# Optimization experiments

Hardware: AMD Instinct MI355X
Metric: run time of the kernel (lower is better)

## Reference

```python
import jax, jax.numpy as jnp
import numpy as np

B, N, F, H, R = 16, 64, 64, 4, 50
C = F * H  # n_coefficients = n_heads * hidden_features
CUTOFF = 5.0  # ExpNormalSmearing cutoff_upper (cutoff_lower = 0)


def _dense(k, fin, fout):
    s = 1.0 / np.sqrt(fin)
    return jax.random.uniform(k, (fin, fout), jnp.float32, -s, s)


def setup_inputs() -> dict:
    key = jax.random.key(0)
    ks = jax.random.split(key, 20)
    start = float(np.exp(-CUTOFF))
    return {
        "h": jax.random.normal(ks[0], (B, N, F), jnp.float32),
        "x": jax.random.normal(ks[1], (B, N, 3), jnp.float32),
        "v": jax.random.normal(ks[2], (B, N, 3), jnp.float32) * 0.1,
        # edge model (ContinuousFilterConvolutionWithConcatenation)
        "W_in": _dense(ks[3], 2 * F, R), "b_in": jnp.zeros((R,), jnp.float32),
        "rbf_means": jnp.linspace(start, 1.0, R).astype(jnp.float32),
        "rbf_betas": jnp.full((R,), (2.0 / R * (1.0 - start)) ** -2, jnp.float32),
        "W_e1": _dense(ks[4], 2 * F + R + 1, F), "b_e1": jnp.zeros((F,), jnp.float32),
        "W_e2": _dense(ks[5], F, F), "b_e2": jnp.zeros((F,), jnp.float32),
        # semantic attention
        "W_sem": _dense(ks[6], F, H), "b_sem": jnp.zeros((H,), jnp.float32),
        "log_gamma": -jnp.log(jnp.linspace(1.0, 5.0, H)).astype(jnp.float32),
        # spatial attention
        "W_xmix": _dense(ks[7], C, C),
        "W_post1": _dense(ks[8], C, F), "b_post1": jnp.zeros((F,), jnp.float32),
        "W_post2": _dense(ks[9], F, F), "b_post2": jnp.zeros((F,), jnp.float32),
        # node update
        "W_node1": _dense(ks[10], F + C + F, F), "b_node1": jnp.zeros((F,), jnp.float32),
        "W_node2": _dense(ks[11], F, F), "b_node2": jnp.zeros((F,), jnp.float32),
        # velocity update
        "W_vel1": _dense(ks[12], F, F), "b_vel1": jnp.zeros((F,), jnp.float32),
        "W_vel2": _dense(ks[13], F, 1),
        "W_vmix": _dense(ks[14], C, 1),
    }


def reference(h, x, v, W_in, b_in, rbf_means, rbf_betas, W_e1, b_e1, W_e2, b_e2,
              W_sem, b_sem, log_gamma, W_xmix, W_post1, b_post1, W_post2, b_post2,
              W_node1, b_node1, W_node2, b_node2, W_vel1, b_vel1, W_vel2, W_vmix):
    silu = jax.nn.silu
    n = h.shape[-2]
    # pairwise displacement x_j - x_i : (B, N, N, 3)
    x_minus_xt = x[..., None, :, :] - x[..., :, None, :]
    d = jnp.sqrt(jax.nn.relu((x_minus_xt ** 2).sum(-1, keepdims=True)) + 1e-5)  # (B,N,N,1)
    # pairwise node features [h_j, h_i] : (B, N, N, 2F)
    hj = jnp.broadcast_to(h[..., None, :, :], h.shape[:-2] + (n, n, h.shape[-1]))
    hi = jnp.broadcast_to(h[..., :, None, :], hj.shape)
    h_cat = jnp.concatenate([hj, hi], -1)
    # edge model: RBF-smeared continuous-filter conv with concatenation
    h_mid = h_cat @ W_in + b_in  # (B,N,N,R)
    cut = 0.5 * (jnp.cos(d * (jnp.pi / CUTOFF)) + 1.0) * (d < CUTOFF)
    rbf = cut * jnp.exp(-rbf_betas * (jnp.exp(-d) - rbf_means) ** 2)  # (B,N,N,R)
    h_e = jnp.concatenate([h_cat, rbf * h_mid, d], -1)
    h_e = silu(h_e @ W_e1 + b_e1) @ W_e2 + b_e2  # (B,N,N,F)
    # attentions, softmax over neighbor axis (-2), diagonal masked out
    eye = jnp.eye(n, dtype=h.dtype)[:, :, None]
    sem = jax.nn.celu(h_e @ W_sem + b_sem, alpha=2.0) - 1e5 * eye
    sem = jax.nn.softmax(sem, axis=-2)  # (B,N,N,H)
    euc = jax.nn.softmax(-(d + 1e5 * eye) * jnp.exp(log_gamma), axis=-2)  # (B,N,N,H)
    att = euc * sem
    att = att / att.sum(-2, keepdims=True)
    # per-head attention-weighted edge features, flattened (F outer, H inner)
    h_e_att = (h_e[..., :, None] * att[..., None, :]).reshape(att.shape[:-1] + (F * H,))
    # spatial attention on unit displacement vectors
    coeff = jnp.tanh(h_e_att @ W_xmix)  # (B,N,N,C)
    x_hat = x_minus_xt / (d + 1e-5)
    comb = x_hat[..., None, :] * coeff[..., None]  # (B,N,N,C,3)
    comb_sum = comb.mean(axis=-3)  # mean over neighbors -> (B,N,C,3)
    h_comb = (comb_sum ** 2).sum(-1)  # invariant squared norms (B,N,C)
    h_comb = silu(silu(h_comb @ W_post1 + b_post1) @ W_post2 + b_post2)
    # node update (residual)
    h_agg = h_e_att.sum(axis=-2)  # (B,N,C)
    h_out = h + silu(silu(jnp.concatenate([h, h_agg, h_comb], -1) @ W_node1 + b_node1) @ W_node2 + b_node2)
    # equivariant velocity / coordinate update
    delta_v = jnp.einsum('...ijcd,c->...id', comb, W_vmix[:, 0]) / n  # v_mixing + mean over j
    gate = 2.0 * jax.nn.sigmoid(silu(h_out @ W_vel1 + b_vel1) @ W_vel2)  # double_sigmoid, (B,N,1)
    v_out = delta_v + gate * v
    x_out = x + v_out
    return h_out, x_out, v_out
```

## Files before the change

kernel.cpp:

```cpp
#include <hip/hip_runtime.h>
#include <math.h>

#define NB 16
#define NN 64
#define NF 64
#define NH 4
#define NR 50
#define NC 256

typedef __attribute__((ext_vector_type(8))) short short8;
typedef __attribute__((ext_vector_type(4))) float f32x4;

#define WS_WE1R 0
#define WS_WE2  4096
#define WS_WX   9216
#define WS_PO1  74752
#define WS_NO1  91136
#define WS_PO2  115712
#define WS_NO2  119808
#define WS_VE1  123904
#define MID_F   64000
#define E1_F    (MID_F + 131072)
#define HAGG_F  (E1_F + 131072)
#define COMB_F  (HAGG_F + 262144)
#define BS2_F   (COMB_F + 786432)

__device__ __forceinline__ float siluf(float x) { return x / (1.f + __expf(-x)); }
__device__ __forceinline__ float tanhfast(float x) { return 1.f - 2.f / (__expf(2.f * x) + 1.f); }

__device__ __forceinline__ short f2bfs(float f) {
    __bf16 b = (__bf16)f;
    union { __bf16 b; short s; } u; u.b = b; return u.s;
}
__device__ __forceinline__ float bf1(ushort u) {
    union { unsigned u; float f; } c; c.u = ((unsigned)u) << 16; return c.f;
}
__device__ __forceinline__ float bflo(unsigned u) {
    union { unsigned u; float f; } c; c.u = u << 16; return c.f;
}
__device__ __forceinline__ float bfhi(unsigned u) {
    union { unsigned u; float f; } c; c.u = u & 0xFFFF0000u; return c.f;
}

__global__ __launch_bounds__(256)
void prep_kernel(const float* __restrict__ W_e1, const float* __restrict__ b_e1,
                 const float* __restrict__ W_e2, const float* __restrict__ b_e2,
                 const float* __restrict__ W_sem, const float* __restrict__ b_sem,
                 const float* __restrict__ W_xmix,
                 const float* __restrict__ W_post1, const float* __restrict__ W_node1,
                 const float* __restrict__ W_post2, const float* __restrict__ W_node2,
                 const float* __restrict__ W_vel1,
                 const float* __restrict__ h, const float* __restrict__ W_in,
                 const float* __restrict__ b_in,
                 short* __restrict__ wpack, float* __restrict__ mid,
                 float* __restrict__ e1, float* __restrict__ bs2)
{
    int blk = blockIdx.x, t = threadIdx.x;
    if (blk < 63) {
        int s = blk * 256 + t;
        if (s >= 16000) return;
        short8 val;
        if (s < 512) {
            int cl = s & 15, g = (s >> 4) & 3, q = s >> 6;
            int ks = q & 1, nt = q >> 1;
            int c = nt * 16 + cl, k0 = 32 * ks + 8 * g;
#pragma unroll
            for (int i = 0; i < 8; i++) {
                int kr = k0 + i;
                float f = (kr < 50) ? W_e1[(128 + kr) * NF + c] : (kr == 50 ? W_e1[178 * NF + c] : 0.f);
                val[i] = f2bfs(f);
            }
            *(short8*)(&wpack[WS_WE1R + s * 8]) = val;
        } else if (s < 1152) {
            int u = s - 512;
            int cl = u & 15, g = (u >> 4) & 3, q = u >> 6;
            int ks = q & 1, nt = q >> 1;
            int c = nt * 16 + cl, k0 = 32 * ks + 8 * g;
#pragma unroll
            for (int i = 0; i < 8; i++) {
                int k = k0 + i;
                float f;
                if (c < 64) f = W_e2[k * NF + c];
                else {
                    int cc = c - 64;
                    if (cc < 4) {
                        f = 0.f;
                        for (int m = 0; m < 64; m++) f += W_e2[k * NF + m] * W_sem[m * NH + cc];
                    } else f = 0.f;
                }
                val[i] = f2bfs(f);
            }
            *(short8*)(&wpack[WS_WE2 + u * 8]) = val;
        } else if (s < 9344) {
            int u = s - 1152;
            int cl = u & 15, g = (u >> 4) & 3, q = u >> 6;
            int ks = q & 7, wn = q >> 3;
            int c = (wn >> 2) * 64 + (wn & 3) * 16 + cl, k0 = 32 * ks + 8 * g;
#pragma unroll
            for (int i = 0; i < 8; i++) val[i] = f2bfs(W_xmix[(k0 + i) * NC + c]);
            *(short8*)(&wpack[WS_WX + u * 8]) = val;
        } else if (s < 11392) {
            int u = s - 9344;
            int cl = u & 15, g = (u >> 4) & 3, q = u >> 6;
            int ks = q & 7, nt = q >> 3;
            int c = nt * 16 + cl, k0 = 32 * ks + 8 * g;
#pragma unroll
            for (int i = 0; i < 8; i++) val[i] = f2bfs(W_post1[(k0 + i) * NF + c]);
            *(short8*)(&wpack[WS_PO1 + u * 8]) = val;
        } else if (s < 14464) {
            int u = s - 11392;
            int cl = u & 15, g = (u >> 4) & 3, q = u >> 6;
            int ks = q % 12, nt = q / 12;
            int c = nt * 16 + cl, k0 = 32 * ks + 8 * g;
#pragma unroll
            for (int i = 0; i < 8; i++) val[i] = f2bfs(W_node1[(k0 + i) * NF + c]);
            *(short8*)(&wpack[WS_NO1 + u * 8]) = val;
        } else if (s < 14976) {
            int u = s - 14464;
            int cl = u & 15, g = (u >> 4) & 3, q = u >> 6;
            int ks = q & 1, nt = q >> 1;
            int c = nt * 16 + cl, k0 = 32 * ks + 8 * g;
#pragma unroll
            for (int i = 0; i < 8; i++) val[i] = f2bfs(W_post2[(k0 + i) * NF + c]);
            *(short8*)(&wpack[WS_PO2 + u * 8]) = val;
        } else if (s < 15488) {
            int u = s - 14976;
            int cl = u & 15, g = (u >> 4) & 3, q = u >> 6;
            int ks = q & 1, nt = q >> 1;
            int c = nt * 16 + cl, k0 = 32 * ks + 8 * g;
#pragma unroll
            for (int i = 0; i < 8; i++) val[i] = f2bfs(W_node2[(k0 + i) * NF + c]);
            *(short8*)(&wpack[WS_NO2 + u * 8]) = val;
        } else {
            int u = s - 15488;
            int cl = u & 15, g = (u >> 4) & 3, q = u >> 6;
            int ks = q & 1, nt = q >> 1;
            int c = nt * 16 + cl, k0 = 32 * ks + 8 * g;
#pragma unroll
            for (int i = 0; i < 8; i++) val[i] = f2bfs(W_vel1[(k0 + i) * NF + c]);
            *(short8*)(&wpack[WS_VE1 + u * 8]) = val;
        }
    } else if (blk == 63) {
        if (t < 4) {
            float acc = b_sem[t];
            for (int m = 0; m < 64; m++) acc += b_e2[m] * W_sem[m * NH + t];
            bs2[t] = acc;
        }
    } else {
        int node = blk - 64;
        __shared__ float s_hn[64];
        if (t < 64) s_hn[t] = h[node * NF + t];
        __syncthreads();
        if (t < 64) {
            float acc = 0.f;
#pragma unroll 8
            for (int k = 0; k < 64; k++) acc += s_hn[k] * W_e1[k * NF + t];
            e1[node * 128 + t] = acc;
        } else if (t < 128) {
            int f = t - 64;
            float acc = b_e1[f];
#pragma unroll 8
            for (int k = 0; k < 64; k++) acc += s_hn[k] * W_e1[(64 + k) * NF + f];
            e1[node * 128 + 64 + f] = acc;
        } else if (t < 178) {
            int r = t - 128;
            float acc = 0.f;
#pragma unroll 8
            for (int k = 0; k < 64; k++) acc += s_hn[k] * W_in[k * NR + r];
            mid[node * 128 + r] = acc;
        } else if (t >= 192 && t < 242) {
            int r = t - 192;
            float acc = b_in[r];
#pragma unroll 8
            for (int k = 0; k < 64; k++) acc += s_hn[k] * W_in[(64 + k) * NR + r];
            mid[node * 128 + 64 + r] = acc;
        }
    }
}

__global__ __launch_bounds__(64)
void sake_edge_kernel(
    const float* __restrict__ x,
    const float* __restrict__ mid, const float* __restrict__ e1,
    const float* __restrict__ rbf_means, const float* __restrict__ rbf_betas,
    const float* __restrict__ b_e2, const float* __restrict__ bs2,
    const float* __restrict__ log_gamma,
    const short* __restrict__ wpack,
    float* __restrict__ hagg_g, float* __restrict__ comb_g)
{
    const int bi = blockIdx.x;
    const int b  = bi >> 6;
    const int i  = bi & 63;
    const int l  = threadIdx.x;
    const int lr = l & 15, lg = l >> 4;

    __shared__ __align__(16) short s_Ar[8 * 64 * 8];
    __shared__ __align__(16) short s_Au[8 * 64 * 8];
    __shared__ __align__(16) short s_he[64 * 72];
    __shared__ float s_xhat[256];
    __shared__ float s_att[256];

    const short8* A8r  = (const short8*)s_Ar;
    short8*       A8rw = (short8*)s_Ar;
    const short8* A8u  = (const short8*)s_Au;
    const short8* We1p = (const short8*)(wpack + WS_WE1R);
    const short8* We2p = (const short8*)(wpack + WS_WE2);
    const short8* Wxp  = (const short8*)(wpack + WS_WX);

    {
        int j = l;
        float dx = x[(b * NN + j) * 3 + 0] - x[(b * NN + i) * 3 + 0];
        float dy = x[(b * NN + j) * 3 + 1] - x[(b * NN + i) * 3 + 1];
        float dz = x[(b * NN + j) * 3 + 2] - x[(b * NN + i) * 3 + 2];
        float d2 = dx * dx + dy * dy + dz * dz;
        float d  = sqrtf(fmaxf(d2, 0.f) + 1e-5f);
        float inv = 1.f / (d + 1e-5f);
        float4 xh = { dx * inv, dy * inv, dz * inv, d };
        *(float4*)(s_xhat + j * 4) = xh;

        float cut = 0.5f * (__cosf(d * 0.6283185307179586f) + 1.f) * (d < 5.f ? 1.f : 0.f);
        float emd = __expf(-d);
        const float* mj = mid + (size_t)(b * 64 + j) * 128;
        const float* mi = mid + (size_t)(b * 64 + i) * 128 + 64;
#pragma unroll
        for (int g = 0; g < 8; g++) {
            short8 val;
#pragma unroll
            for (int e = 0; e < 8; e++) {
                int r = g * 8 + e;
                float o;
                if (r < 50) {
                    float m = mj[r] + mi[r];
                    float df = emd - rbf_means[r];
                    o = cut * __expf(-rbf_betas[r] * df * df) * m;
                } else if (r == 50) o = d;
                else o = 0.f;
                val[e] = f2bfs(o);
            }
            A8rw[g * 64 + j] = val;
        }
    }

    {
        const float* e1b = e1 + (size_t)b * 64 * 128;
        float e1iv[4];
#pragma unroll
        for (int nt = 0; nt < 4; nt++) e1iv[nt] = e1b[i * 128 + 64 + nt * 16 + lr];
        f32x4 accU[4][4];
#pragma unroll
        for (int jt = 0; jt < 4; jt++)
#pragma unroll
            for (int nt = 0; nt < 4; nt++) {
                int f = nt * 16 + lr;
#pragma unroll
                for (int r = 0; r < 4; r++) {
                    int j = jt * 16 + lg * 4 + r;
                    accU[jt][nt][r] = e1b[j * 128 + f] + e1iv[nt];
                }
            }
#pragma unroll
        for (int ks = 0; ks < 2; ks++) {
            short8 aa[4];
#pragma unroll
            for (int jt = 0; jt < 4; jt++) aa[jt] = A8r[(ks * 4 + lg) * 64 + jt * 16 + lr];
#pragma unroll
            for (int nt = 0; nt < 4; nt++) {
                short8 bb = We1p[(nt * 2 + ks) * 64 + l];
#pragma unroll
                for (int jt = 0; jt < 4; jt++)
                    accU[jt][nt] = __builtin_amdgcn_mfma_f32_16x16x32_bf16(aa[jt], bb, accU[jt][nt], 0, 0, 0);
            }
        }
#pragma unroll
        for (int jt = 0; jt < 4; jt++)
#pragma unroll
            for (int nt = 0; nt < 4; nt++) {
                int f = nt * 16 + lr;
#pragma unroll
                for (int r = 0; r < 4; r++) {
                    int j = jt * 16 + lg * 4 + r;
                    s_Au[((f >> 3) * 64 + j) * 8 + (f & 7)] = f2bfs(siluf(accU[jt][nt][r]));
                }
            }
    }

    f32x4 accS[4];
    {
        f32x4 accE[4][4];
#pragma unroll
        for (int jt = 0; jt < 4; jt++) {
            accS[jt][0] = 0.f; accS[jt][1] = 0.f; accS[jt][2] = 0.f; accS[jt][3] = 0.f;
#pragma unroll
            for (int nt = 0; nt < 4; nt++) {
                accE[jt][nt][0] = 0.f; accE[jt][nt][1] = 0.f; accE[jt][nt][2] = 0.f; accE[jt][nt][3] = 0.f;
            }
        }
#pragma unroll
        for (int ks = 0; ks < 2; ks++) {
            short8 aa[4];
#pragma unroll
            for (int jt = 0; jt < 4; jt++) aa[jt] = A8u[(ks * 4 + lg) * 64 + jt * 16 + lr];
            short8 bb2 = We2p[(8 + ks) * 64 + l];
#pragma unroll
            for (int jt = 0; jt < 4; jt++)
                accS[jt] = __builtin_amdgcn_mfma_f32_16x16x32_bf16(aa[jt], bb2, accS[jt], 0, 0, 0);
#pragma unroll
            for (int nt = 0; nt < 4; nt++) {
                short8 bb = We2p[(nt * 2 + ks) * 64 + l];
#pragma unroll
                for (int jt = 0; jt < 4; jt++)
                    accE[jt][nt] = __builtin_amdgcn_mfma_f32_16x16x32_bf16(aa[jt], bb, accE[jt][nt], 0, 0, 0);
            }
        }
        float be2v[4];
#pragma unroll
        for (int nt = 0; nt < 4; nt++) be2v[nt] = b_e2[nt * 16 + lr];
#pragma unroll
        for (int jt = 0; jt < 4; jt++)
#pragma unroll
            for (int nt = 0; nt < 4; nt++) {
                int f = nt * 16 + lr;
#pragma unroll
                for (int r = 0; r < 4; r++) {
                    int j = jt * 16 + lg * 4 + r;
                    s_he[j * 72 + f] = f2bfs(accE[jt][nt][r] + be2v[nt]);
                }
            }
    }

    {
        float gam = __expf(log_gamma[lr & 3]);
        float bsv = bs2[lr & 3];
        float cel[4][4], dj[4][4];
        float m1 = -1e30f, m2 = -1e30f;
#pragma unroll
        for (int jt = 0; jt < 4; jt++)
#pragma unroll
            for (int r = 0; r < 4; r++) {
                int j = jt * 16 + lg * 4 + r;
                float s = accS[jt][r] + bsv;
                float c = fmaxf(s, 0.f) + fminf(0.f, 2.f * (__expf(0.5f * s) - 1.f));
                float d = s_xhat[j * 4 + 3];
                if (j == i) { c -= 1e5f; d += 1e5f; }
                cel[jt][r] = c; dj[jt][r] = d;
                m1 = fmaxf(m1, c);
                m2 = fmaxf(m2, -d * gam);
            }
        m1 = fmaxf(m1, __shfl_xor(m1, 16)); m1 = fmaxf(m1, __shfl_xor(m1, 32));
        m2 = fmaxf(m2, __shfl_xor(m2, 16)); m2 = fmaxf(m2, __shfl_xor(m2, 32));
        float at[4][4];
        float S1 = 0.f, S2 = 0.f;
#pragma unroll
        for (int jt = 0; jt < 4; jt++)
#pragma unroll
            for (int r = 0; r < 4; r++) {
                float ev1 = __expf(cel[jt][r] - m1);
                float ev2 = __expf(-dj[jt][r] * gam - m2);
                cel[jt][r] = ev1; dj[jt][r] = ev2;
                S1 += ev1; S2 += ev2;
            }
        S1 += __shfl_xor(S1, 16); S1 += __shfl_xor(S1, 32);
        S2 += __shfl_xor(S2, 16); S2 += __shfl_xor(S2, 32);
        float S3 = 0.f;
        float inv12 = 1.f / (S1 * S2);
#pragma unroll
        for (int jt = 0; jt < 4; jt++)
#pragma unroll
            for (int r = 0; r < 4; r++) {
                at[jt][r] = cel[jt][r] * dj[jt][r] * inv12;
                S3 += at[jt][r];
            }
        S3 += __shfl_xor(S3, 16); S3 += __shfl_xor(S3, 32);
        float inv3 = 1.f / S3;
        if (lr < 4) {
#pragma unroll
            for (int jt = 0; jt < 4; jt++)
#pragma unroll
                for (int r = 0; r < 4; r++) {
                    int j = jt * 16 + lg * 4 + r;
                    s_att[j * 4 + lr] = at[jt][r] * inv3;
                }
        }
    }

    {
        float hg0 = 0.f, hg1 = 0.f, hg2 = 0.f, hg3 = 0.f;
#pragma unroll 8
        for (int j = 0; j < 64; j++) {
            float hev = bf1((ushort)s_he[j * 72 + l]);
            float4 at = *(const float4*)(s_att + j * 4);
            hg0 += hev * at.x; hg1 += hev * at.y; hg2 += hev * at.z; hg3 += hev * at.w;
        }
        float4 o = { hg0, hg1, hg2, hg3 };
        *(float4*)(hagg_g + bi * 256 + l * 4) = o;
    }

    {
        short8 fr[4][8];
#pragma unroll
        for (int jt = 0; jt < 4; jt++) {
            int j = jt * 16 + lr;
            float4 a = *(const float4*)(s_att + j * 4);
#pragma unroll
            for (int ks = 0; ks < 8; ks++) {
                unsigned hv = *(const unsigned*)(s_he + j * 72 + ks * 8 + lg * 2);
                float h0 = bflo(hv), h1 = bfhi(hv);
                short8 v;
                v[0] = f2bfs(h0 * a.x); v[1] = f2bfs(h0 * a.y);
                v[2] = f2bfs(h0 * a.z); v[3] = f2bfs(h0 * a.w);
                v[4] = f2bfs(h1 * a.x); v[5] = f2bfs(h1 * a.y);
                v[6] = f2bfs(h1 * a.z); v[7] = f2bfs(h1 * a.w);
                fr[jt][ks] = v;
            }
        }
#pragma unroll 1
        for (int nq = 0; nq < 4; nq++) {
            f32x4 acc[4][4];
#pragma unroll
            for (int jt = 0; jt < 4; jt++)
#pragma unroll
                for (int nt = 0; nt < 4; nt++) {
                    acc[jt][nt][0] = 0.f; acc[jt][nt][1] = 0.f;
                    acc[jt][nt][2] = 0.f; acc[jt][nt][3] = 0.f;
                }
#pragma unroll
            for (int ks = 0; ks < 8; ks++) {
#pragma unroll
                for (int nt = 0; nt < 4; nt++) {
                    short8 bb = Wxp[((nq * 4 + nt) * 8 + ks) * 64 + l];
#pragma unroll
                    for (int jt = 0; jt < 4; jt++)
                        acc[jt][nt] = __builtin_amdgcn_mfma_f32_16x16x32_bf16(fr[jt][ks], bb, acc[jt][nt], 0, 0, 0);
                }
            }
            float p[4][3];
#pragma unroll
            for (int nt = 0; nt < 4; nt++) { p[nt][0] = 0.f; p[nt][1] = 0.f; p[nt][2] = 0.f; }
#pragma unroll
            for (int jt = 0; jt < 4; jt++) {
#pragma unroll
                for (int r = 0; r < 4; r++) {
                    int j = jt * 16 + lg * 4 + r;
                    float4 xh = *(const float4*)(s_xhat + j * 4);
#pragma unroll
                    for (int nt = 0; nt < 4; nt++) {
                        float th = tanhfast(acc[jt][nt][r]);
                        p[nt][0] += xh.x * th;
                        p[nt][1] += xh.y * th;
                        p[nt][2] += xh.z * th;
                    }
                }
            }
#pragma unroll
            for (int nt = 0; nt < 4; nt++) {
#pragma unroll
                for (int k = 0; k < 3; k++) {
                    float val = p[nt][k];
                    val += __shfl_xor(val, 16);
                    val += __shfl_xor(val, 32);
                    if (lg == 0)
                        comb_g[bi * 768 + (nq * 64 + nt * 16 + lr) * 3 + k] = val * (1.f / 64.f);
                }
            }
        }
    }
}

__global__ __launch_bounds__(256)
void sake_tail_kernel(
    const float* __restrict__ h, const float* __restrict__ x, const float* __restrict__ v,
    const float* __restrict__ hagg_g, const float* __restrict__ comb_g,
    const float* __restrict__ b_post1, const float* __restrict__ b_post2,
    const float* __restrict__ b_node1, const float* __restrict__ b_node2,
    const float* __restrict__ b_vel1,
    const float* __restrict__ W_vel2, const float* __restrict__ W_vmix,
    const short* __restrict__ wpack,
    float* __restrict__ out_h, float* __restrict__ out_x, float* __restrict__ out_v)
{
    const int g0 = blockIdx.x * 16;
    const int t = threadIdx.x;
    const int w = t >> 6, l = t & 63, lr = l & 15, lg = l >> 4;

    __shared__ __align__(16) short s_Aa[88 * 16 * 8];
    __shared__ float s_wv[256];
    __shared__ float s_wv2[64];
    __shared__ float s_red[4][16];

    const short8* A8  = (const short8*)s_Aa;
    const short8* PO1p = (const short8*)(wpack + WS_PO1);
    const short8* NO1p = (const short8*)(wpack + WS_NO1);
    const short8* PO2p = (const short8*)(wpack + WS_PO2);
    const short8* NO2p = (const short8*)(wpack + WS_NO2);
    const short8* VE1p = (const short8*)(wpack + WS_VE1);

    {
        s_wv[t] = W_vmix[t];
        if (t < 64) s_wv2[t] = W_vel2[t];
        int n = t & 15, c0 = (t >> 4) * 16;
        const float* cg = comb_g + (g0 + n) * 768;
        const float* ha = hagg_g + (g0 + n) * 256;
#pragma unroll
        for (int cc = 0; cc < 16; cc++) {
            int c = c0 + cc;
            float v0 = cg[c * 3 + 0], v1 = cg[c * 3 + 1], v2 = cg[c * 3 + 2];
            float hcp = v0 * v0 + v1 * v1 + v2 * v2;
            s_Aa[((c >> 3) * 16 + n) * 8 + (c & 7)] = f2bfs(hcp);
            s_Aa[((40 + (c >> 3)) * 16 + n) * 8 + (c & 7)] = f2bfs(ha[c]);
        }
        int f0 = (t >> 4) * 4;
#pragma unroll
        for (int ff = 0; ff < 4; ff++) {
            int f = f0 + ff;
            s_Aa[((32 + (f >> 3)) * 16 + n) * 8 + (f & 7)] = f2bfs(h[(g0 + n) * 64 + f]);
        }
    }
    __syncthreads();

    {
        f32x4 acc = {0.f, 0.f, 0.f, 0.f};
#pragma unroll
        for (int ks = 0; ks < 8; ks++) {
            short8 aa = A8[(ks * 4 + lg) * 16 + lr];
            short8 bb = PO1p[((w * 8 + ks) * 4 + lg) * 16 + lr];
            acc = __builtin_amdgcn_mfma_f32_16x16x32_bf16(aa, bb, acc, 0, 0, 0);
        }
        int f = w * 16 + lr;
        float bp = b_post1[f];
        __syncthreads();
#pragma unroll
        for (int r = 0; r < 4; r++) {
            int n = lg * 4 + r;
            s_Aa[((80 + (f >> 3)) * 16 + n) * 8 + (f & 7)] = f2bfs(siluf(acc[r] + bp));
        }
        __syncthreads();
    }
    {
        f32x4 acc = {0.f, 0.f, 0.f, 0.f};
#pragma unroll
        for (int ks = 0; ks < 2; ks++) {
            short8 aa = A8[((80 + ks * 4 + lg)) * 16 + lr];
            short8 bb = PO2p[((w * 2 + ks) * 4 + lg) * 16 + lr];
            acc = __builtin_amdgcn_mfma_f32_16x16x32_bf16(aa, bb, acc, 0, 0, 0);
        }
        int f = w * 16 + lr;
        float bp = b_post2[f];
#pragma unroll
        for (int r = 0; r < 4; r++) {
            int n = lg * 4 + r;
            s_Aa[((72 + (f >> 3)) * 16 + n) * 8 + (f & 7)] = f2bfs(siluf(acc[r] + bp));
        }
        __syncthreads();
    }
    {
        f32x4 acc = {0.f, 0.f, 0.f, 0.f};
#pragma unroll
        for (int ks = 0; ks < 12; ks++) {
            short8 aa = A8[((32 + ks * 4 + lg)) * 16 + lr];
            short8 bb = NO1p[((w * 12 + ks) * 4 + lg) * 16 + lr];
            acc = __builtin_amdgcn_mfma_f32_16x16x32_bf16(aa, bb, acc, 0, 0, 0);
        }
        int f = w * 16 + lr;
        float bp = b_node1[f];
#pragma unroll
        for (int r = 0; r < 4; r++) {
            int n = lg * 4 + r;
            s_Aa[((f >> 3) * 16 + n) * 8 + (f & 7)] = f2bfs(siluf(acc[r] + bp));
        }
        __syncthreads();
    }
    {
        f32x4 acc = {0.f, 0.f, 0.f, 0.f};
#pragma unroll
        for (int ks = 0; ks < 2; ks++) {
            short8 aa = A8[(ks * 4 + lg) * 16 + lr];
            short8 bb = NO2p[((w * 2 + ks) * 4 + lg) * 16 + lr];
            acc = __builtin_amdgcn_mfma_f32_16x16x32_bf16(aa, bb, acc, 0, 0, 0);
        }
        int f = w * 16 + lr;
        float bp = b_node2[f];
#pragma unroll
        for (int r = 0; r < 4; r++) {
            int n = lg * 4 + r;
            float ho = h[(g0 + n) * 64 + f] + siluf(acc[r] + bp);
            out_h[(g0 + n) * 64 + f] = ho;
            s_Aa[((8 + (f >> 3)) * 16 + n) * 8 + (f & 7)] = f2bfs(ho);
        }
        __syncthreads();
    }
    {
        f32x4 acc = {0.f, 0.f, 0.f, 0.f};
#pragma unroll
        for (int ks = 0; ks < 2; ks++) {
            short8 aa = A8[((8 + ks * 4 + lg)) * 16 + lr];
            short8 bb = VE1p[((w * 2 + ks) * 4 + lg) * 16 + lr];
            acc = __builtin_amdgcn_mfma_f32_16x16x32_bf16(aa, bb, acc, 0, 0, 0);
        }
        int f = w * 16 + lr;
        float bp = b_vel1[f];
        float wv2 = s_wv2[f];
#pragma unroll
        for (int r = 0; r < 4; r++) {
            float pv = siluf(acc[r] + bp) * wv2;
            pv += __shfl_xor(pv, 1); pv += __shfl_xor(pv, 2);
            pv += __shfl_xor(pv, 4); pv += __shfl_xor(pv, 8);
            if (lr == 0) s_red[w][lg * 4 + r] = pv;
        }
        __syncthreads();
    }
    {
        int n = t >> 4, qq = t & 15;
        float p0 = 0.f, p1 = 0.f, p2 = 0.f;
        const float* cg = comb_g + (g0 + n) * 768;
#pragma unroll
        for (int cc = 0; cc < 16; cc++) {
            int c = qq * 16 + cc;
            float wv = s_wv[c];
            p0 += cg[c * 3 + 0] * wv;
            p1 += cg[c * 3 + 1] * wv;
            p2 += cg[c * 3 + 2] * wv;
        }
        p0 += __shfl_xor(p0, 1); p0 += __shfl_xor(p0, 2); p0 += __shfl_xor(p0, 4); p0 += __shfl_xor(p0, 8);
        p1 += __shfl_xor(p1, 1); p1 += __shfl_xor(p1, 2); p1 += __shfl_xor(p1, 4); p1 += __shfl_xor(p1, 8);
        p2 += __shfl_xor(p2, 1); p2 += __shfl_xor(p2, 2); p2 += __shfl_xor(p2, 4); p2 += __shfl_xor(p2, 8);
        if (qq == 0) {
            float g = s_red[0][n] + s_red[1][n] + s_red[2][n] + s_red[3][n];
            g = 2.f / (1.f + __expf(-g));
            float dv0 = p0 + g * v[(g0 + n) * 3 + 0];
            float dv1 = p1 + g * v[(g0 + n) * 3 + 1];
            float dv2 = p2 + g * v[(g0 + n) * 3 + 2];
            out_v[(g0 + n) * 3 + 0] = dv0;
            out_v[(g0 + n) * 3 + 1] = dv1;
            out_v[(g0 + n) * 3 + 2] = dv2;
            out_x[(g0 + n) * 3 + 0] = x[(g0 + n) * 3 + 0] + dv0;
            out_x[(g0 + n) * 3 + 1] = x[(g0 + n) * 3 + 1] + dv1;
            out_x[(g0 + n) * 3 + 2] = x[(g0 + n) * 3 + 2] + dv2;
        }
    }
}

extern "C" void kernel_launch(void* const* d_in, const int* in_sizes, int n_in,
                              void* d_out, int out_size, void* d_ws, size_t ws_size,
                              hipStream_t stream) {
    const float* h        = (const float*)d_in[0];
    const float* x        = (const float*)d_in[1];
    const float* v        = (const float*)d_in[2];
    const float* W_in     = (const float*)d_in[3];
    const float* b_in     = (const float*)d_in[4];
    const float* rbf_m    = (const float*)d_in[5];
    const float* rbf_b    = (const float*)d_in[6];
    const float* W_e1     = (const float*)d_in[7];
    const float* b_e1     = (const float*)d_in[8];
    const float* W_e2     = (const float*)d_in[9];
    const float* b_e2     = (const float*)d_in[10];
    const float* W_sem    = (const float*)d_in[11];
    const float* b_sem    = (const float*)d_in[12];
    const float* log_g    = (const float*)d_in[13];
    const float* W_xmix   = (const float*)d_in[14];
    const float* W_post1  = (const float*)d_in[15];
    const float* b_post1  = (const float*)d_in[16];
    const float* W_post2  = (const float*)d_in[17];
    const float* b_post2  = (const float*)d_in[18];
    const float* W_node1  = (const float*)d_in[19];
    const float* b_node1  = (const float*)d_in[20];
    const float* W_node2  = (const float*)d_in[21];
    const float* b_node2  = (const float*)d_in[22];
    const float* W_vel1   = (const float*)d_in[23];
    const float* b_vel1   = (const float*)d_in[24];
    const float* W_vel2   = (const float*)d_in[25];
    const float* W_vmix   = (const float*)d_in[26];

    float* out   = (float*)d_out;
    float* out_h = out;
    float* out_x = out + NB * NN * NF;
    float* out_v = out + NB * NN * NF + NB * NN * 3;

    short* wpack = (short*)d_ws;
    float* wsf   = (float*)d_ws;
    float* mid   = wsf + MID_F;
    float* e1    = wsf + E1_F;
    float* hagg  = wsf + HAGG_F;
    float* comb  = wsf + COMB_F;
    float* bs2   = wsf + BS2_F;

    prep_kernel<<<64 + 1024, 256, 0, stream>>>(
        W_e1, b_e1, W_e2, b_e2, W_sem, b_sem, W_xmix,
        W_post1, W_node1, W_post2, W_node2, W_vel1,
        h, W_in, b_in, wpack, mid, e1, bs2);

    sake_edge_kernel<<<NB * NN, 64, 0, stream>>>(
        x, mid, e1, rbf_m, rbf_b, b_e2, bs2, log_g,
        wpack, hagg, comb);

    sake_tail_kernel<<<64, 256, 0, stream>>>(
        h, x, v, hagg, comb,
        b_post1, b_post2, b_node1, b_node2, b_vel1,
        W_vel2, W_vmix, wpack, out_h, out_x, out_v);
}
```

Before: 59.08 us.

## Split edge kernel across four waves and repack W_xmix per head

The edge kernel grows from one 64-thread wave to four waves per (batch, node) block. Each wave owns a 16-column slice of the edge MLP outputs and a 64-column slice of the xmix GEMM. The W_xmix packing is reorganized by head so A fragments are built per head, which cuts per-wave register pressure. The comb output layout changes to component-major (planar xyz) and the tail kernel reads it accordingly. This adds block-level syncs and has only wave 0 compute the semantic attention, leaving the other waves idle during that step.

Result: slower. 60.91 us (+3.1%).

```diff
diff --git a/kernel.cpp b/kernel.cpp
--- a/kernel.cpp
+++ b/kernel.cpp
@@ -82,22 +82,21 @@
                 float f;
                 if (c < 64) f = W_e2[k * NF + c];
                 else {
-                    int cc = c - 64;
-                    if (cc < 4) {
-                        f = 0.f;
-                        for (int m = 0; m < 64; m++) f += W_e2[k * NF + m] * W_sem[m * NH + cc];
-                    } else f = 0.f;
+                    int cc = (c - 64) & 3;
+                    f = 0.f;
+                    for (int m = 0; m < 64; m++) f += W_e2[k * NF + m] * W_sem[m * NH + cc];
                 }
                 val[i] = f2bfs(f);
             }
             *(short8*)(&wpack[WS_WE2 + u * 8]) = val;
         } else if (s < 9344) {
             int u = s - 1152;
-            int cl = u & 15, g = (u >> 4) & 3, q = u >> 6;
-            int ks = q & 7, wn = q >> 3;
-            int c = (wn >> 2) * 64 + (wn & 3) * 16 + cl, k0 = 32 * ks + 8 * g;
-#pragma unroll
-            for (int i = 0; i < 8; i++) val[i] = f2bfs(W_xmix[(k0 + i) * NC + c]);
+            int l2 = u & 63, ks = (u >> 6) & 1, hh = (u >> 7) & 3, ct = u >> 9;
+            int lr2 = l2 & 15, lg2 = l2 >> 4;
+            int c = ct * 16 + lr2, k0 = ks * 32 + lg2 * 8;
+#pragma unroll
+            for (int i = 0; i < 8; i++)
+                val[i] = f2bfs(W_xmix[((k0 + i) * 4 + hh) * NC + c]);
             *(short8*)(&wpack[WS_WX + u * 8]) = val;
         } else if (s < 11392) {
             int u = s - 9344;
@@ -178,7 +177,7 @@
     }
 }
 
-__global__ __launch_bounds__(64)
+__global__ __launch_bounds__(256)
 void sake_edge_kernel(
     const float* __restrict__ x,
     const float* __restrict__ mid, const float* __restrict__ e1,
@@ -191,276 +190,263 @@
     const int bi = blockIdx.x;
     const int b  = bi >> 6;
     const int i  = bi & 63;
-    const int l  = threadIdx.x;
-    const int lr = l & 15, lg = l >> 4;
-
-    __shared__ __align__(16) short s_Ar[8 * 64 * 8];
-    __shared__ __align__(16) short s_Au[8 * 64 * 8];
+    const int t  = threadIdx.x;
+    const int w  = t >> 6, l = t & 63, lr = l & 15, lg = l >> 4;
+
+    __shared__ __align__(16) short s_A[16 * 64 * 8];
     __shared__ __align__(16) short s_he[64 * 72];
     __shared__ float s_xhat[256];
     __shared__ float s_att[256];
-
-    const short8* A8r  = (const short8*)s_Ar;
-    short8*       A8rw = (short8*)s_Ar;
-    const short8* A8u  = (const short8*)s_Au;
+    __shared__ float s_midi[52];
+
+    const short8* A8  = (const short8*)s_A;
+    short8*       A8w = (short8*)s_A;
     const short8* We1p = (const short8*)(wpack + WS_WE1R);
     const short8* We2p = (const short8*)(wpack + WS_WE2);
     const short8* Wxp  = (const short8*)(wpack + WS_WX);
 
-    {
-        int j = l;
+    if (t < 50) s_midi[t] = mid[(b * 64 + i) * 128 + 64 + t];
+    if (t < 64) {
+        int j = t;
         float dx = x[(b * NN + j) * 3 + 0] - x[(b * NN + i) * 3 + 0];
         float dy = x[(b * NN + j) * 3 + 1] - x[(b * NN + i) * 3 + 1];
         float dz = x[(b * NN + j) * 3 + 2] - x[(b * NN + i) * 3 + 2];
         float d2 = dx * dx + dy * dy + dz * dz;
         float d  = sqrtf(fmaxf(d2, 0.f) + 1e-5f);
         float inv = 1.f / (d + 1e-5f);
-        float4 xh = { dx * inv, dy * inv, dz * inv, d };
-        *(float4*)(s_xhat + j * 4) = xh;
-
+        s_xhat[j * 4 + 0] = dx * inv;
+        s_xhat[j * 4 + 1] = dy * inv;
+        s_xhat[j * 4 + 2] = dz * inv;
+        s_xhat[j * 4 + 3] = d;
+    }
+    __syncthreads();
+
+    const int fW = w * 16 + lr;
+    const float* e1b = e1 + (size_t)b * 64 * 128;
+    float e1i_v = e1b[i * 128 + 64 + fW];
+    float e1v[4][4];
+#pragma unroll
+    for (int jt = 0; jt < 4; jt++)
+#pragma unroll
+        for (int r = 0; r < 4; r++)
+            e1v[jt][r] = e1b[(jt * 16 + lg * 4 + r) * 128 + fW];
+    float be2 = b_e2[fW];
+    float gam = __expf(log_gamma[lr & 3]);
+    float bsv = bs2[lr & 3];
+
+    {
+        int j = t & 63, p = t >> 6;
+        float d = s_xhat[j * 4 + 3];
         float cut = 0.5f * (__cosf(d * 0.6283185307179586f) + 1.f) * (d < 5.f ? 1.f : 0.f);
         float emd = __expf(-d);
         const float* mj = mid + (size_t)(b * 64 + j) * 128;
-        const float* mi = mid + (size_t)(b * 64 + i) * 128 + 64;
-#pragma unroll
-        for (int g = 0; g < 8; g++) {
+#pragma unroll
+        for (int q = 0; q < 2; q++) {
+            int sl = 2 * p + q;
             short8 val;
 #pragma unroll
             for (int e = 0; e < 8; e++) {
-                int r = g * 8 + e;
+                int r = sl * 8 + e;
                 float o;
                 if (r < 50) {
-                    float m = mj[r] + mi[r];
+                    float m = mj[r] + s_midi[r];
                     float df = emd - rbf_means[r];
                     o = cut * __expf(-rbf_betas[r] * df * df) * m;
                 } else if (r == 50) o = d;
                 else o = 0.f;
                 val[e] = f2bfs(o);
             }
-            A8rw[g * 64 + j] = val;
-        }
-    }
-
-    {
-        const float* e1b = e1 + (size_t)b * 64 * 128;
-        float e1iv[4];
-#pragma unroll
-        for (int nt = 0; nt < 4; nt++) e1iv[nt] = e1b[i * 128 + 64 + nt * 16 + lr];
-        f32x4 accU[4][4];
+            A8w[sl * 64 + j] = val;
+        }
+    }
+    __syncthreads();
+
+    {
+        f32x4 acc[4];
 #pragma unroll
         for (int jt = 0; jt < 4; jt++)
 #pragma unroll
-            for (int nt = 0; nt < 4; nt++) {
-                int f = nt * 16 + lr;
+            for (int r = 0; r < 4; r++) acc[jt][r] = e1v[jt][r] + e1i_v;
+#pragma unroll
+        for (int ks = 0; ks < 2; ks++) {
+            short8 bb = We1p[(w * 2 + ks) * 64 + l];
+#pragma unroll
+            for (int jt = 0; jt < 4; jt++) {
+                short8 aa = A8[(ks * 4 + lg) * 64 + jt * 16 + lr];
+                acc[jt] = __builtin_amdgcn_mfma_f32_16x16x32_bf16(aa, bb, acc[jt], 0, 0, 0);
+            }
+        }
+#pragma unroll
+        for (int jt = 0; jt < 4; jt++)
+#pragma unroll
+            for (int r = 0; r < 4; r++) {
+                int j = jt * 16 + lg * 4 + r;
+                s_A[(((fW >> 3) + 8) * 64 + j) * 8 + (fW & 7)] = f2bfs(siluf(acc[jt][r]));
+            }
+        __syncthreads();
+    }
+
+    {
+        f32x4 accE[4], accS[4];
+#pragma unroll
+        for (int jt = 0; jt < 4; jt++) {
+            accE[jt][0] = 0.f; accE[jt][1] = 0.f; accE[jt][2] = 0.f; accE[jt][3] = 0.f;
+            accS[jt][0] = 0.f; accS[jt][1] = 0.f; accS[jt][2] = 0.f; accS[jt][3] = 0.f;
+        }
+#pragma unroll
+        for (int ks = 0; ks < 2; ks++) {
+            short8 aa[4];
+#pragma unroll
+            for (int jt = 0; jt < 4; jt++) aa[jt] = A8[(8 + ks * 4 + lg) * 64 + jt * 16 + lr];
+            short8 bb = We2p[(w * 2 + ks) * 64 + l];
+#pragma unroll
+            for (int jt = 0; jt < 4; jt++)
+                accE[jt] = __builtin_amdgcn_mfma_f32_16x16x32_bf16(aa[jt], bb, accE[jt], 0, 0, 0);
+            if (w == 0) {
+                short8 bb2 = We2p[(8 + ks) * 64 + l];
+#pragma unroll
+                for (int jt = 0; jt < 4; jt++)
+                    accS[jt] = __builtin_amdgcn_mfma_f32_16x16x32_bf16(aa[jt], bb2, accS[jt], 0, 0, 0);
+            }
+        }
+#pragma unroll
+        for (int jt = 0; jt < 4; jt++)
+#pragma unroll
+            for (int r = 0; r < 4; r++) {
+                int j = jt * 16 + lg * 4 + r;
+                s_he[j * 72 + fW] = f2bfs(accE[jt][r] + be2);
+            }
+        if (w == 0) {
+            float cel[4][4], dj[4][4];
+            float m1 = -1e30f, m2 = -1e30f;
+#pragma unroll
+            for (int jt = 0; jt < 4; jt++)
 #pragma unroll
                 for (int r = 0; r < 4; r++) {
                     int j = jt * 16 + lg * 4 + r;
-                    accU[jt][nt][r] = e1b[j * 128 + f] + e1iv[nt];
+                    float s = accS[jt][r] + bsv;
+                    float c = fmaxf(s, 0.f) + fminf(0.f, 2.f * (__expf(0.5f * s) - 1.f));
+                    float d = s_xhat[j * 4 + 3];
+                    if (j == i) { c -= 1e5f; d += 1e5f; }
+                    cel[jt][r] = c; dj[jt][r] = d;
+                    m1 = fmaxf(m1, c);
+                    m2 = fmaxf(m2, -d * gam);
                 }
-            }
-#pragma unroll
-        for (int ks = 0; ks < 2; ks++) {
-            short8 aa[4];
-#pragma unroll
-            for (int jt = 0; jt < 4; jt++) aa[jt] = A8r[(ks * 4 + lg) * 64 + jt * 16 + lr];
-#pragma unroll
-            for (int nt = 0; nt < 4; nt++) {
-                short8 bb = We1p[(nt * 2 + ks) * 64 + l];
+            m1 = fmaxf(m1, __shfl_xor(m1, 16)); m1 = fmaxf(m1, __shfl_xor(m1, 32));
+            m2 = fmaxf(m2, __shfl_xor(m2, 16)); m2 = fmaxf(m2, __shfl_xor(m2, 32));
+            float S1 = 0.f, S2 = 0.f;
+#pragma unroll
+            for (int jt = 0; jt < 4; jt++)
+#pragma unroll
+                for (int r = 0; r < 4; r++) {
+                    float ev1 = __expf(cel[jt][r] - m1);
+                    float ev2 = __expf(-dj[jt][r] * gam - m2);
+                    cel[jt][r] = ev1; dj[jt][r] = ev2;
+                    S1 += ev1; S2 += ev2;
+                }
+            S1 += __shfl_xor(S1, 16); S1 += __shfl_xor(S1, 32);
+            S2 += __shfl_xor(S2, 16); S2 += __shfl_xor(S2, 32);
+            float inv12 = 1.f / (S1 * S2);
+            float at[4][4];
+            float S3 = 0.f;
+#pragma unroll
+            for (int jt = 0; jt < 4; jt++)
+#pragma unroll
+                for (int r = 0; r < 4; r++) {
+                    at[jt][r] = cel[jt][r] * dj[jt][r] * inv12;
+                    S3 += at[jt][r];
+                }
+            S3 += __shfl_xor(S3, 16); S3 += __shfl_xor(S3, 32);
+            float inv3 = 1.f / S3;
+            if (lr < 4) {
 #pragma unroll
                 for (int jt = 0; jt < 4; jt++)
-                    accU[jt][nt] = __builtin_amdgcn_mfma_f32_16x16x32_bf16(aa[jt], bb, accU[jt][nt], 0, 0, 0);
-            }
-        }
+#pragma unroll
+                    for (int r = 0; r < 4; r++) {
+                        int j = jt * 16 + lg * 4 + r;
+                        s_att[j * 4 + lr] = at[jt][r] * inv3;
+                    }
+            }
+        }
+        __syncthreads();
+    }
+
+    {
+        int f2 = t >> 3, hh = (t >> 1) & 3, jh = t & 1;
+        float a0 = 0.f, a1 = 0.f;
+#pragma unroll 8
+        for (int jj = 0; jj < 32; jj++) {
+            int j = jh * 32 + jj;
+            float at = s_att[j * 4 + hh];
+            unsigned u = *(const unsigned*)(s_he + j * 72 + 2 * f2);
+            a0 += bflo(u) * at;
+            a1 += bfhi(u) * at;
+        }
+        a0 += __shfl_xor(a0, 1);
+        a1 += __shfl_xor(a1, 1);
+        if (!jh) {
+            hagg_g[bi * 256 + (2 * f2) * 4 + hh]     = a0;
+            hagg_g[bi * 256 + (2 * f2 + 1) * 4 + hh] = a1;
+        }
+    }
+
+    {
+        f32x4 acc[4][4];
 #pragma unroll
         for (int jt = 0; jt < 4; jt++)
 #pragma unroll
-            for (int nt = 0; nt < 4; nt++) {
-                int f = nt * 16 + lr;
-#pragma unroll
-                for (int r = 0; r < 4; r++) {
-                    int j = jt * 16 + lg * 4 + r;
-                    s_Au[((f >> 3) * 64 + j) * 8 + (f & 7)] = f2bfs(siluf(accU[jt][nt][r]));
+            for (int ct = 0; ct < 4; ct++) {
+                acc[jt][ct][0] = 0.f; acc[jt][ct][1] = 0.f;
+                acc[jt][ct][2] = 0.f; acc[jt][ct][3] = 0.f;
+            }
+#pragma unroll 1
+        for (int h = 0; h < 4; h++) {
+            float ah[4];
+#pragma unroll
+            for (int jt = 0; jt < 4; jt++) ah[jt] = s_att[(jt * 16 + lr) * 4 + h];
+#pragma unroll
+            for (int ks = 0; ks < 2; ks++) {
+                short8 fr[4];
+#pragma unroll
+                for (int jt = 0; jt < 4; jt++) {
+                    short8 he8 = *(const short8*)(s_he + (jt * 16 + lr) * 72 + ks * 32 + lg * 8);
+                    short8 v;
+#pragma unroll
+                    for (int e = 0; e < 8; e++) v[e] = f2bfs(bf1((ushort)he8[e]) * ah[jt]);
+                    fr[jt] = v;
                 }
-            }
-    }
-
-    f32x4 accS[4];
-    {
-        f32x4 accE[4][4];
-#pragma unroll
-        for (int jt = 0; jt < 4; jt++) {
-            accS[jt][0] = 0.f; accS[jt][1] = 0.f; accS[jt][2] = 0.f; accS[jt][3] = 0.f;
-#pragma unroll
-            for (int nt = 0; nt < 4; nt++) {
-                accE[jt][nt][0] = 0.f; accE[jt][nt][1] = 0.f; accE[jt][nt][2] = 0.f; accE[jt][nt][3] = 0.f;
-            }
-        }
-#pragma unroll
-        for (int ks = 0; ks < 2; ks++) {
-            short8 aa[4];
-#pragma unroll
-            for (int jt = 0; jt < 4; jt++) aa[jt] = A8u[(ks * 4 + lg) * 64 + jt * 16 + lr];
-            short8 bb2 = We2p[(8 + ks) * 64 + l];
+#pragma unroll
+                for (int ct = 0; ct < 4; ct++) {
+                    short8 bb = Wxp[(((w * 4 + ct) * 4 + h) * 2 + ks) * 64 + l];
+#pragma unroll
+                    for (int jt = 0; jt < 4; jt++)
+                        acc[jt][ct] = __builtin_amdgcn_mfma_f32_16x16x32_bf16(fr[jt], bb, acc[jt][ct], 0, 0, 0);
+                }
+            }
+        }
+        float* cgb = comb_g + bi * 768;
+#pragma unroll
+        for (int ct = 0; ct < 4; ct++) {
+            float p0 = 0.f, p1 = 0.f, p2 = 0.f;
 #pragma unroll
             for (int jt = 0; jt < 4; jt++)
-                accS[jt] = __builtin_amdgcn_mfma_f32_16x16x32_bf16(aa[jt], bb2, accS[jt], 0, 0, 0);
-#pragma unroll
-            for (int nt = 0; nt < 4; nt++) {
-                short8 bb = We2p[(nt * 2 + ks) * 64 + l];
-#pragma unroll
-                for (int jt = 0; jt < 4; jt++)
-                    accE[jt][nt] = __builtin_amdgcn_mfma_f32_16x16x32_bf16(aa[jt], bb, accE[jt][nt], 0, 0, 0);
-            }
-        }
-        float be2v[4];
-#pragma unroll
-        for (int nt = 0; nt < 4; nt++) be2v[nt] = b_e2[nt * 16 + lr];
-#pragma unroll
-        for (int jt = 0; jt < 4; jt++)
-#pragma unroll
-            for (int nt = 0; nt < 4; nt++) {
-                int f = nt * 16 + lr;
-#pragma unroll
-                for (int r = 0; r < 4; r++) {
-                    int j = jt * 16 + lg * 4 + r;
-                    s_he[j * 72 + f] = f2bfs(accE[jt][nt][r] + be2v[nt]);
-                }
-            }
-    }
-
-    {
-        float gam = __expf(log_gamma[lr & 3]);
-        float bsv = bs2[lr & 3];
-        float cel[4][4], dj[4][4];
-        float m1 = -1e30f, m2 = -1e30f;
-#pragma unroll
-        for (int jt = 0; jt < 4; jt++)
-#pragma unroll
-            for (int r = 0; r < 4; r++) {
-                int j = jt * 16 + lg * 4 + r;
-                float s = accS[jt][r] + bsv;
-                float c = fmaxf(s, 0.f) + fminf(0.f, 2.f * (__expf(0.5f * s) - 1.f));
-                float d = s_xhat[j * 4 + 3];
-                if (j == i) { c -= 1e5f; d += 1e5f; }
-                cel[jt][r] = c; dj[jt][r] = d;
-                m1 = fmaxf(m1, c);
-                m2 = fmaxf(m2, -d * gam);
-            }
-        m1 = fmaxf(m1, __shfl_xor(m1, 16)); m1 = fmaxf(m1, __shfl_xor(m1, 32));
-        m2 = fmaxf(m2, __shfl_xor(m2, 16)); m2 = fmaxf(m2, __shfl_xor(m2, 32));
-        float at[4][4];
-        float S1 = 0.f, S2 = 0.f;
-#pragma unroll
-        for (int jt = 0; jt < 4; jt++)
-#pragma unroll
-            for (int r = 0; r < 4; r++) {
-                float ev1 = __expf(cel[jt][r] - m1);
-                float ev2 = __expf(-dj[jt][r] * gam - m2);
-                cel[jt][r] = ev1; dj[jt][r] = ev2;
-                S1 += ev1; S2 += ev2;
-            }
-        S1 += __shfl_xor(S1, 16); S1 += __shfl_xor(S1, 32);
-        S2 += __shfl_xor(S2, 16); S2 += __shfl_xor(S2, 32);
-        float S3 = 0.f;
-        float inv12 = 1.f / (S1 * S2);
-#pragma unroll
-        for (int jt = 0; jt < 4; jt++)
-#pragma unroll
-            for (int r = 0; r < 4; r++) {
-                at[jt][r] = cel[jt][r] * dj[jt][r] * inv12;
-                S3 += at[jt][r];
-            }
-        S3 += __shfl_xor(S3, 16); S3 += __shfl_xor(S3, 32);
-        float inv3 = 1.f / S3;
-        if (lr < 4) {
-#pragma unroll
-            for (int jt = 0; jt < 4; jt++)
-#pragma unroll
-                for (int r = 0; r < 4; r++) {
-                    int j = jt * 16 + lg * 4 + r;
-                    s_att[j * 4 + lr] = at[jt][r] * inv3;
-                }
-        }
-    }
-
-    {
-        float hg0 = 0.f, hg1 = 0.f, hg2 = 0.f, hg3 = 0.f;
-#pragma unroll 8
-        for (int j = 0; j < 64; j++) {
-            float hev = bf1((ushort)s_he[j * 72 + l]);
-            float4 at = *(const float4*)(s_att + j * 4);
-            hg0 += hev * at.x; hg1 += hev * at.y; hg2 += hev * at.z; hg3 += hev * at.w;
-        }
-        float4 o = { hg0, hg1, hg2, hg3 };
-        *(float4*)(hagg_g + bi * 256 + l * 4) = o;
-    }
-
-    {
-        short8 fr[4][8];
-#pragma unroll
-        for (int jt = 0; jt < 4; jt++) {
-            int j = jt * 16 + lr;
-            float4 a = *(const float4*)(s_att + j * 4);
-#pragma unroll
-            for (int ks = 0; ks < 8; ks++) {
-                unsigned hv = *(const unsigned*)(s_he + j * 72 + ks * 8 + lg * 2);
-                float h0 = bflo(hv), h1 = bfhi(hv);
-                short8 v;
-                v[0] = f2bfs(h0 * a.x); v[1] = f2bfs(h0 * a.y);
-                v[2] = f2bfs(h0 * a.z); v[3] = f2bfs(h0 * a.w);
-                v[4] = f2bfs(h1 * a.x); v[5] = f2bfs(h1 * a.y);
-                v[6] = f2bfs(h1 * a.z); v[7] = f2bfs(h1 * a.w);
-                fr[jt][ks] = v;
-            }
-        }
-#pragma unroll 1
-        for (int nq = 0; nq < 4; nq++) {
-            f32x4 acc[4][4];
-#pragma unroll
-            for (int jt = 0; jt < 4; jt++)
-#pragma unroll
-                for (int nt = 0; nt < 4; nt++) {
-                    acc[jt][nt][0] = 0.f; acc[jt][nt][1] = 0.f;
-                    acc[jt][nt][2] = 0.f; acc[jt][nt][3] = 0.f;
-                }
-#pragma unroll
-            for (int ks = 0; ks < 8; ks++) {
-#pragma unroll
-                for (int nt = 0; nt < 4; nt++) {
-                    short8 bb = Wxp[((nq * 4 + nt) * 8 + ks) * 64 + l];
-#pragma unroll
-                    for (int jt = 0; jt < 4; jt++)
-                        acc[jt][nt] = __builtin_amdgcn_mfma_f32_16x16x32_bf16(fr[jt][ks], bb, acc[jt][nt], 0, 0, 0);
-                }
-            }
-            float p[4][3];
-#pragma unroll
-            for (int nt = 0; nt < 4; nt++) { p[nt][0] = 0.f; p[nt][1] = 0.f; p[nt][2] = 0.f; }
-#pragma unroll
-            for (int jt = 0; jt < 4; jt++) {
 #pragma unroll
                 for (int r = 0; r < 4; r++) {
                     int j = jt * 16 + lg * 4 + r;
                     float4 xh = *(const float4*)(s_xhat + j * 4);
-#pragma unroll
-                    for (int nt = 0; nt < 4; nt++) {
-                        float th = tanhfast(acc[jt][nt][r]);
-                        p[nt][0] += xh.x * th;
-                        p[nt][1] += xh.y * th;
-                        p[nt][2] += xh.z * th;
-                    }
+                    float th = tanhfast(acc[jt][ct][r]);
+                    p0 += xh.x * th;
+                    p1 += xh.y * th;
+                    p2 += xh.z * th;
                 }
-            }
-#pragma unroll
-            for (int nt = 0; nt < 4; nt++) {
-#pragma unroll
-                for (int k = 0; k < 3; k++) {
-                    float val = p[nt][k];
-                    val += __shfl_xor(val, 16);
-                    val += __shfl_xor(val, 32);
-                    if (lg == 0)
-                        comb_g[bi * 768 + (nq * 64 + nt * 16 + lr) * 3 + k] = val * (1.f / 64.f);
-                }
+            p0 += __shfl_xor(p0, 16); p0 += __shfl_xor(p0, 32);
+            p1 += __shfl_xor(p1, 16); p1 += __shfl_xor(p1, 32);
+            p2 += __shfl_xor(p2, 16); p2 += __shfl_xor(p2, 32);
+            if (lg == 0) {
+                int c = (w * 4 + ct) * 16 + lr;
+                cgb[c]       = p0 * (1.f / 64.f);
+                cgb[256 + c] = p1 * (1.f / 64.f);
+                cgb[512 + c] = p2 * (1.f / 64.f);
             }
         }
     }
@@ -502,7 +488,7 @@
 #pragma unroll
         for (int cc = 0; cc < 16; cc++) {
             int c = c0 + cc;
-            float v0 = cg[c * 3 + 0], v1 = cg[c * 3 + 1], v2 = cg[c * 3 + 2];
+            float v0 = cg[c], v1 = cg[256 + c], v2 = cg[512 + c];
             float hcp = v0 * v0 + v1 * v1 + v2 * v2;
             s_Aa[((c >> 3) * 16 + n) * 8 + (c & 7)] = f2bfs(hcp);
             s_Aa[((40 + (c >> 3)) * 16 + n) * 8 + (c & 7)] = f2bfs(ha[c]);
@@ -615,9 +601,9 @@
         for (int cc = 0; cc < 16; cc++) {
             int c = qq * 16 + cc;
             float wv = s_wv[c];
-            p0 += cg[c * 3 + 0] * wv;
-            p1 += cg[c * 3 + 1] * wv;
-            p2 += cg[c * 3 + 2] * wv;
+            p0 += cg[c] * wv;
+            p1 += cg[256 + c] * wv;
+            p2 += cg[512 + c] * wv;
         }
         p0 += __shfl_xor(p0, 1); p0 += __shfl_xor(p0, 2); p0 += __shfl_xor(p0, 4); p0 += __shfl_xor(p0, 8);
         p1 += __shfl_xor(p1, 1); p1 += __shfl_xor(p1, 2); p1 += __shfl_xor(p1, 4); p1 += __shfl_xor(p1, 8);
@@ -687,7 +673,7 @@
         W_post1, W_node1, W_post2, W_node2, W_vel1,
         h, W_in, b_in, wpack, mid, e1, bs2);
 
-    sake_edge_kernel<<<NB * NN, 64, 0, stream>>>(
+    sake_edge_kernel<<<NB * NN, 256, 0, stream>>>(
         x, mid, e1, rbf_m, rbf_b, b_e2, bs2, log_g,
         wpack, hagg, comb);
 
```
